# Optimization experiments

Hardware: AMD Instinct MI355X
Metric: run time of the kernel (lower is better)

## Reference

```python
import jax, jax.numpy as jnp
import numpy as np

IN_F = 128
OUT_F = 64
ALPHA = 0.2  # LeakyReLU slope for attention logits
NEG_INF = -9e15


def setup_inputs() -> dict:
    key = jax.random.key(0)
    k1, k2, k3, k4 = jax.random.split(key, 4)
    B, N = 4, 2048
    h = jax.random.normal(k1, (B, N, IN_F), dtype=jnp.float32)
    adj = jax.random.randint(k2, (B, N, N), 0, 2, dtype=jnp.int32)
    # xavier_uniform with gain=1.414
    def xavier(k, shape, gain=1.414):
        fan_in, fan_out = shape[0], shape[1]
        bound = gain * np.sqrt(6.0 / (fan_in + fan_out))
        return jax.random.uniform(k, shape, jnp.float32, -bound, bound)
    W = xavier(k3, (IN_F, OUT_F))
    a = xavier(k4, (2 * OUT_F, 1))
    return {"h": h, "adj": adj, "W": W, "a": a}


def reference(h, adj, W, a):
    # Wh: [B, N, F_out]
    Wh = jnp.einsum("bnf,fo->bno", h, W)
    # e_ij = LeakyReLU(a_left . Wh_i + a_right . Wh_j), avoiding the
    # O(N^2 * 2F) concatenated tensor the torch code materializes.
    a_l = a[:OUT_F, 0]   # [F_out]
    a_r = a[OUT_F:, 0]   # [F_out]
    e_l = Wh @ a_l       # [B, N]
    e_r = Wh @ a_r       # [B, N]
    e = jax.nn.leaky_relu(e_l[:, :, None] + e_r[:, None, :], ALPHA)  # [B,N,N]
    masked = jnp.where(adj > 0, e, NEG_INF)
    attention = jax.nn.softmax(masked, axis=2)
    # dropout p=0.0 (eval-mode / deterministic) -> identity
    h_prime = jax.nn.leaky_relu(jnp.einsum("bij,bjo->bio", attention, Wh), 0.01)
    return (h_prime, attention)
```

## Files before the change

kernel.cpp:

```cpp
#include <hip/hip_runtime.h>

#define NN 2048
#define BB 4
#define IN_F 128
#define OUT_F 64

typedef __attribute__((ext_vector_type(8))) short short8;
typedef __attribute__((ext_vector_type(4))) float f32x4;
typedef __attribute__((ext_vector_type(4))) int i32x4;

__device__ __forceinline__ ushort f2bf(float f) {
  uint u = __float_as_uint(f);
  uint r = (u + 0x7fffu + ((u >> 16) & 1u)) >> 16;
  return (ushort)r;
}
__device__ __forceinline__ float bf2f(ushort s) {
  return __uint_as_float(((uint)s) << 16);
}

__global__ __launch_bounds__(64) void wh_el_er_kernel(
    const float* __restrict__ h, const float* __restrict__ W,
    const float* __restrict__ a, ushort* __restrict__ Whbf,
    float* __restrict__ el, float* __restrict__ er) {
  int row = blockIdx.x;
  int o = threadIdx.x;
  const float* hr = h + (size_t)row * IN_F;
  float wh = 0.f;
  #pragma unroll 8
  for (int f = 0; f < IN_F; ++f) wh += hr[f] * W[f * OUT_F + o];
  Whbf[(size_t)row * OUT_F + o] = f2bf(wh);
  float vl = wh * a[o];
  float vr = wh * a[OUT_F + o];
  #pragma unroll
  for (int d = 32; d > 0; d >>= 1) {
    vl += __shfl_down(vl, d);
    vr += __shfl_down(vr, d);
  }
  if (o == 0) { el[row] = vl; er[row] = vr; }
}

__global__ __launch_bounds__(256) void transpose_kernel(
    const ushort* __restrict__ Whbf, ushort* __restrict__ WhbfT) {
  __shared__ uint tile[64][65];
  int b = blockIdx.x >> 5;
  int j0 = (blockIdx.x & 31) << 6;
  int t = threadIdx.x;
  int o = t & 63, jg = t >> 6;
  #pragma unroll
  for (int m = 0; m < 16; ++m) {
    int jj = jg * 16 + m;
    tile[jj][o] = (uint)Whbf[((size_t)(b * NN + j0 + jj)) * OUT_F + o];
  }
  __syncthreads();
  int oo = t >> 2, grp = t & 3;
  uint out[8];
  #pragma unroll
  for (int m = 0; m < 16; m += 2) {
    uint u0 = tile[grp * 16 + m][oo];
    uint u1 = tile[grp * 16 + m + 1][oo];
    out[m >> 1] = u0 | (u1 << 16);
  }
  uint4* dst = (uint4*)(WhbfT + ((size_t)(b * OUT_F + oo)) * NN + j0 + grp * 16);
  dst[0] = *(uint4*)&out[0];
  dst[1] = *(uint4*)&out[4];
}

__global__ __launch_bounds__(512, 4) void attn_kernel(
    const int* __restrict__ adj, const ushort* __restrict__ WhbfT,
    const float* __restrict__ el, const float* __restrict__ er,
    float* __restrict__ attn_out, float* __restrict__ hprime) {
  __shared__ __align__(16) char pbuf[16 * 4096];
  __shared__ float ers[NN];
  __shared__ float sinv[16];

  int blk = blockIdx.x;
  int b = blk >> 7;
  int i0 = (blk & 127) << 4;
  int tid = threadIdx.x;
  int wave = tid >> 6, lane = tid & 63;

  ((f32x4*)ers)[tid] = ((const f32x4*)(er + (size_t)b * NN))[tid];
  __syncthreads();

  int r0 = wave * 2, r1 = r0 + 1;
  int ia = i0 + r0, ib = i0 + r1;
  float el0 = el[(size_t)b * NN + ia];
  float el1 = el[(size_t)b * NN + ib];
  const i32x4* arow0 = (const i32x4*)(adj + ((size_t)(b * NN + ia)) * NN);
  const i32x4* arow1 = (const i32x4*)(adj + ((size_t)(b * NN + ib)) * NN);

  i32x4 a0[8], a1[8];
  #pragma unroll
  for (int it = 0; it < 8; ++it) {
    a0[it] = __builtin_nontemporal_load(&arow0[lane + 64 * it]);
    a1[it] = __builtin_nontemporal_load(&arow1[lane + 64 * it]);
  }

  uint2 pva0[8], pva1[8];
  float ss0 = 0.f, ss1 = 0.f;
  #pragma unroll
  for (int it = 0; it < 8; ++it) {
    f32x4 ev = *(const f32x4*)&ers[(lane + 64 * it) * 4];
    float evv[4] = {ev.x, ev.y, ev.z, ev.w};
    int   av0[4] = {a0[it].x, a0[it].y, a0[it].z, a0[it].w};
    int   av1[4] = {a1[it].x, a1[it].y, a1[it].z, a1[it].w};
    float pe0[4], pe1[4];
    #pragma unroll
    for (int k = 0; k < 4; ++k) {
      float e0 = el0 + evv[k];
      e0 = fmaxf(e0, 0.2f * e0);
      float x0 = __expf(e0);
      pe0[k] = av0[k] > 0 ? x0 : 0.f;
      ss0 += pe0[k];
      float e1 = el1 + evv[k];
      e1 = fmaxf(e1, 0.2f * e1);
      float x1 = __expf(e1);
      pe1[k] = av1[k] > 0 ? x1 : 0.f;
      ss1 += pe1[k];
    }
    uint2 w0, w1;
    w0.x = (uint)f2bf(pe0[0]) | ((uint)f2bf(pe0[1]) << 16);
    w0.y = (uint)f2bf(pe0[2]) | ((uint)f2bf(pe0[3]) << 16);
    w1.x = (uint)f2bf(pe1[0]) | ((uint)f2bf(pe1[1]) << 16);
    w1.y = (uint)f2bf(pe1[2]) | ((uint)f2bf(pe1[3]) << 16);
    pva0[it] = w0;
    pva1[it] = w1;
  }
  #pragma unroll
  for (int d = 32; d > 0; d >>= 1) {
    ss0 += __shfl_xor(ss0, d);
    ss1 += __shfl_xor(ss1, d);
  }
  if (lane == 0) { sinv[r0] = 1.f / ss0; sinv[r1] = 1.f / ss1; }

  {
    char* lr0 = pbuf + r0 * 4096;
    char* lr1 = pbuf + r1 * 4096;
    int sw0 = (r0 & 7) << 4, sw1 = (r1 & 7) << 4;
    #pragma unroll
    for (int it = 0; it < 8; ++it) {
      *(uint2*)(lr0 + (((lane + 64 * it) * 8) ^ sw0)) = pva0[it];
      *(uint2*)(lr1 + (((lane + 64 * it) * 8) ^ sw1)) = pva1[it];
    }
  }
  __syncthreads();

  if (wave < 4) {
    int o0 = wave * 16;
    int lo16 = lane & 15, hi4 = lane >> 4;
    const char* prowA = pbuf + lo16 * 4096;
    int swA = (lo16 & 7) << 4;
    const ushort* brow = WhbfT + ((size_t)(b * OUT_F + o0 + lo16)) * NN;

    f32x4 acc0 = {0.f, 0.f, 0.f, 0.f};
    f32x4 acc1 = {0.f, 0.f, 0.f, 0.f};
    #pragma unroll 8
    for (int kk = 0; kk < 32; ++kk) {
      int ka = kk * 32 + hi4 * 8;
      int kb = ka + 1024;
      short8 af0 = *(const short8*)(prowA + ((ka * 2) ^ swA));
      short8 bf0 = *(const short8*)(brow + ka);
      acc0 = __builtin_amdgcn_mfma_f32_16x16x32_bf16(af0, bf0, acc0, 0, 0, 0);
      short8 af1 = *(const short8*)(prowA + ((kb * 2) ^ swA));
      short8 bf1 = *(const short8*)(brow + kb);
      acc1 = __builtin_amdgcn_mfma_f32_16x16x32_bf16(af1, bf1, acc1, 0, 0, 0);
    }
    #pragma unroll
    for (int q = 0; q < 4; ++q) {
      int crow = hi4 * 4 + q;
      float v = (acc0[q] + acc1[q]) * sinv[crow];
      v = v > 0.f ? v : 0.01f * v;
      hprime[((size_t)(b * NN + i0 + crow)) * OUT_F + o0 + lo16] = v;
    }
  } else {
    #pragma unroll
    for (int m = 0; m < 4; ++m) {
      int r = (wave - 4) * 4 + m;
      float inv = sinv[r];
      const char* lr = pbuf + r * 4096;
      int sw = (r & 7) << 4;
      f32x4* orow = (f32x4*)(attn_out + ((size_t)(b * NN + i0 + r)) * NN);
      #pragma unroll
      for (int it = 0; it < 8; ++it) {
        uint2 w2 = *(const uint2*)(lr + (((lane + 64 * it) * 8) ^ sw));
        f32x4 v;
        v.x = bf2f((ushort)(w2.x & 0xffff)) * inv;
        v.y = bf2f((ushort)(w2.x >> 16)) * inv;
        v.z = bf2f((ushort)(w2.y & 0xffff)) * inv;
        v.w = bf2f((ushort)(w2.y >> 16)) * inv;
        orow[lane + 64 * it] = v;
      }
    }
  }
}

extern "C" void kernel_launch(void* const* d_in, const int* in_sizes, int n_in,
                              void* d_out, int out_size, void* d_ws, size_t ws_size,
                              hipStream_t stream) {
  const float* h  = (const float*)d_in[0];
  const int* adj  = (const int*)d_in[1];
  const float* W  = (const float*)d_in[2];
  const float* a  = (const float*)d_in[3];

  float* hprime   = (float*)d_out;
  float* attn_out = (float*)d_out + (size_t)BB * NN * OUT_F;

  ushort* Whbf  = (ushort*)d_ws;
  ushort* WhbfT = Whbf + (size_t)BB * NN * OUT_F;
  float* el = (float*)(WhbfT + (size_t)BB * OUT_F * NN);
  float* er = el + (size_t)BB * NN;

  hipLaunchKernelGGL(wh_el_er_kernel, dim3(BB * NN), dim3(64), 0, stream,
                     h, W, a, Whbf, el, er);
  hipLaunchKernelGGL(transpose_kernel, dim3(BB * (NN / 64)), dim3(256), 0, stream,
                     Whbf, WhbfT);
  hipLaunchKernelGGL(attn_kernel, dim3(BB * (NN / 16)), dim3(512), 0, stream,
                     adj, WhbfT, el, er, attn_out, hprime);
}
```

Measured before the change: 54.02 us.

## Pack adjacency into bitmask in prep kernel and read bits in attention

The adjacency matrix is now compressed into a 1-bit-per-entry mask inside a merged prep kernel that also computes Wh, el and er. The attention kernel reads 32 bits per lane and spreads the nibbles with shuffles instead of loading int32 rows. The full adjacency read still happens once, but it moves out of the attention kernel, whose register pressure and load latency should drop. The cost is an extra bitmask write/read pass plus shuffle work, and the whole adjacency read now sits in a separate prep stage.

```diff
diff --git a/kernel.cpp b/kernel.cpp
--- a/kernel.cpp
+++ b/kernel.cpp
@@ -18,25 +18,43 @@
   return __uint_as_float(((uint)s) << 16);
 }
 
-__global__ __launch_bounds__(64) void wh_el_er_kernel(
+__global__ __launch_bounds__(256) void prep_kernel(
     const float* __restrict__ h, const float* __restrict__ W,
-    const float* __restrict__ a, ushort* __restrict__ Whbf,
-    float* __restrict__ el, float* __restrict__ er) {
-  int row = blockIdx.x;
-  int o = threadIdx.x;
-  const float* hr = h + (size_t)row * IN_F;
-  float wh = 0.f;
-  #pragma unroll 8
-  for (int f = 0; f < IN_F; ++f) wh += hr[f] * W[f * OUT_F + o];
-  Whbf[(size_t)row * OUT_F + o] = f2bf(wh);
-  float vl = wh * a[o];
-  float vr = wh * a[OUT_F + o];
-  #pragma unroll
-  for (int d = 32; d > 0; d >>= 1) {
-    vl += __shfl_down(vl, d);
-    vr += __shfl_down(vr, d);
-  }
-  if (o == 0) { el[row] = vl; er[row] = vr; }
+    const float* __restrict__ a, const int* __restrict__ adj,
+    ushort* __restrict__ Whbf, float* __restrict__ el,
+    float* __restrict__ er, ushort* __restrict__ bits) {
+  int blk = blockIdx.x;
+  if (blk < 4096) {
+    size_t base = (size_t)blk * 4096;
+    int t = threadIdx.x;
+    const i32x4* src = (const i32x4*)(adj + base) + t * 4;
+    uint bv = 0;
+    #pragma unroll
+    for (int q = 0; q < 4; ++q) {
+      i32x4 v = __builtin_nontemporal_load(&src[q]);
+      bv |= (v.x > 0 ? 1u : 0u) << (q * 4);
+      bv |= (v.y > 0 ? 2u : 0u) << (q * 4);
+      bv |= (v.z > 0 ? 4u : 0u) << (q * 4);
+      bv |= (v.w > 0 ? 8u : 0u) << (q * 4);
+    }
+    bits[base / 16 + t] = (ushort)bv;
+  } else {
+    int row = (blk - 4096) * 4 + (threadIdx.x >> 6);
+    int o = threadIdx.x & 63;
+    const float* hr = h + (size_t)row * IN_F;
+    float wh = 0.f;
+    #pragma unroll 8
+    for (int f = 0; f < IN_F; ++f) wh += hr[f] * W[f * OUT_F + o];
+    Whbf[(size_t)row * OUT_F + o] = f2bf(wh);
+    float vl = wh * a[o];
+    float vr = wh * a[OUT_F + o];
+    #pragma unroll
+    for (int d = 32; d > 0; d >>= 1) {
+      vl += __shfl_down(vl, d);
+      vr += __shfl_down(vr, d);
+    }
+    if (o == 0) { el[row] = vl; er[row] = vr; }
+  }
 }
 
 __global__ __launch_bounds__(256) void transpose_kernel(
@@ -66,7 +84,7 @@
 }
 
 __global__ __launch_bounds__(512, 4) void attn_kernel(
-    const int* __restrict__ adj, const ushort* __restrict__ WhbfT,
+    const ushort* __restrict__ bits, const ushort* __restrict__ WhbfT,
     const float* __restrict__ el, const float* __restrict__ er,
     float* __restrict__ attn_out, float* __restrict__ hprime) {
   __shared__ __align__(16) char pbuf[16 * 4096];
@@ -86,36 +104,30 @@
   int ia = i0 + r0, ib = i0 + r1;
   float el0 = el[(size_t)b * NN + ia];
   float el1 = el[(size_t)b * NN + ib];
-  const i32x4* arow0 = (const i32x4*)(adj + ((size_t)(b * NN + ia)) * NN);
-  const i32x4* arow1 = (const i32x4*)(adj + ((size_t)(b * NN + ib)) * NN);
-
-  i32x4 a0[8], a1[8];
-  #pragma unroll
-  for (int it = 0; it < 8; ++it) {
-    a0[it] = __builtin_nontemporal_load(&arow0[lane + 64 * it]);
-    a1[it] = __builtin_nontemporal_load(&arow1[lane + 64 * it]);
-  }
+  uint wl0 = ((const uint*)bits)[(size_t)(b * NN + ia) * 64 + lane];
+  uint wl1 = ((const uint*)bits)[(size_t)(b * NN + ib) * 64 + lane];
+  int srcbase = lane >> 3, nsh = (lane & 7) * 4;
 
   uint2 pva0[8], pva1[8];
   float ss0 = 0.f, ss1 = 0.f;
   #pragma unroll
   for (int it = 0; it < 8; ++it) {
+    uint n0 = (__shfl(wl0, srcbase + 8 * it) >> nsh) & 0xF;
+    uint n1 = (__shfl(wl1, srcbase + 8 * it) >> nsh) & 0xF;
     f32x4 ev = *(const f32x4*)&ers[(lane + 64 * it) * 4];
     float evv[4] = {ev.x, ev.y, ev.z, ev.w};
-    int   av0[4] = {a0[it].x, a0[it].y, a0[it].z, a0[it].w};
-    int   av1[4] = {a1[it].x, a1[it].y, a1[it].z, a1[it].w};
     float pe0[4], pe1[4];
     #pragma unroll
     for (int k = 0; k < 4; ++k) {
       float e0 = el0 + evv[k];
       e0 = fmaxf(e0, 0.2f * e0);
       float x0 = __expf(e0);
-      pe0[k] = av0[k] > 0 ? x0 : 0.f;
+      pe0[k] = (n0 >> k) & 1 ? x0 : 0.f;
       ss0 += pe0[k];
       float e1 = el1 + evv[k];
       e1 = fmaxf(e1, 0.2f * e1);
       float x1 = __expf(e1);
-      pe1[k] = av1[k] > 0 ? x1 : 0.f;
+      pe1[k] = (n1 >> k) & 1 ? x1 : 0.f;
       ss1 += pe1[k];
     }
     uint2 w0, w1;
@@ -209,11 +221,12 @@
   ushort* WhbfT = Whbf + (size_t)BB * NN * OUT_F;
   float* el = (float*)(WhbfT + (size_t)BB * OUT_F * NN);
   float* er = el + (size_t)BB * NN;
-
-  hipLaunchKernelGGL(wh_el_er_kernel, dim3(BB * NN), dim3(64), 0, stream,
-                     h, W, a, Whbf, el, er);
+  ushort* bits = (ushort*)(er + (size_t)BB * NN);
+
+  hipLaunchKernelGGL(prep_kernel, dim3(4096 + BB * NN / 4), dim3(256), 0, stream,
+                     h, W, a, adj, Whbf, el, er, bits);
   hipLaunchKernelGGL(transpose_kernel, dim3(BB * (NN / 64)), dim3(256), 0, stream,
                      Whbf, WhbfT);
   hipLaunchKernelGGL(attn_kernel, dim3(BB * (NN / 16)), dim3(512), 0, stream,
-                     adj, WhbfT, el, er, attn_out, hprime);
-}
+                     bits, WhbfT, el, er, attn_out, hprime);
+}
```

Result: slower. 66.80 us (+23.7%).
